# Kernel optimization log

Hardware: AMD Instinct MI355X
Metric: run time of the kernel (lower is better)

## Reference

```python
import jax, jax.numpy as jnp
import numpy as np

NEIGHBORS = 16   # K nearest neighbors per query point
NQUERIES = 4096  # number of sampled query points (npts)
B, N = 8, 16384  # batch, points per cloud


def setup_inputs() -> dict:
    key = jax.random.key(0)
    xyz1 = jax.random.normal(key, (B, N, 3), dtype=jnp.float32)
    return {"xyz1": xyz1}


def _sample_one(xyz, key):
    """Sequential coverage sampling for one point cloud xyz: (n, 3).

    Faithful to indices_conv_reduction: a 'used' counter per point; each
    iteration picks a uniformly-random point among the least-used points
    (TF carries current_id and resets it to min(used) when exhausted; since
    counters only increase, this is exactly equivalent to cur = min(used)
    every step), takes its K nearest neighbors, and bumps their counters
    (+1 for neighbors, +100 extra for the chosen center).
    """
    n = xyz.shape[0]

    def step(used, k):
        cur = jnp.min(used)
        mask = used == cur                      # least-used candidate set
        cnt = jnp.sum(mask)
        r = jax.random.randint(k, (), 0, cnt)   # uniform pick among candidates
        index = jnp.argmax(jnp.cumsum(mask) > r)  # r-th True position
        pt = xyz[index]                          # (3,)
        d = jnp.sum((xyz - pt[None, :]) ** 2, axis=1)  # (n,) squared dists
        _, ids = jax.lax.top_k(-d, NEIGHBORS)    # K nearest, sorted
        used = used.at[ids].add(1)
        used = used.at[index].add(100)
        return used, (ids.astype(jnp.int32), pt)

    keys = jax.random.split(key, NQUERIES)
    _, (ids, pts) = jax.lax.scan(step, jnp.zeros((n,), jnp.int32), keys)
    return ids[:, :, None], pts  # (npts, K, 1) int32, (npts, 3) f32


def reference(xyz1):
    xyz1 = jax.lax.stop_gradient(xyz1)  # matches tf.stop_gradient in original
    b = xyz1.shape[0]
    keys = jax.random.split(jax.random.key(42), b)
    idx, pts = jax.vmap(_sample_one)(xyz1, keys)
    return idx, pts
```

## Files before the change

### kernel.cpp

```cpp
#include <hip/hip_runtime.h>
#include <stdint.h>


namespace {

constexpr int BATCH = 8;
constexpr int NPTS  = 16384;
constexpr int NQ    = 4096;
constexpr int KNN   = 16;
constexpr int BLOCK = 512;
constexpr int CH    = NPTS / BLOCK;
constexpr int NWAVE = BLOCK / 64;
constexpr int FLUSH = 256;
constexpr int NCAND = 128;
constexpr size_t IDX_ELEMS = (size_t)BATCH * NQ * KNN;

__device__ __forceinline__ int swz32(int v) { return v + (v >> 5); }
__device__ __forceinline__ int swz16(int w) { return w + 2 * (w >> 6); }

__device__ __forceinline__ void tf2x32(uint32_t k0, uint32_t k1,
                                       uint32_t x0, uint32_t x1,
                                       uint32_t &o0, uint32_t &o1) {
  uint32_t ks2 = k0 ^ k1 ^ 0x1BD11BDAu;
  x0 += k0; x1 += k1;
#define TFR(r) { x0 += x1; x1 = (x1 << (r)) | (x1 >> (32 - (r))); x1 ^= x0; }
  TFR(13) TFR(15) TFR(26) TFR(6)
  x0 += k1;  x1 += ks2 + 1u;
  TFR(17) TFR(29) TFR(16) TFR(24)
  x0 += ks2; x1 += k0 + 2u;
  TFR(13) TFR(15) TFR(26) TFR(6)
  x0 += k0;  x1 += k1 + 3u;
  TFR(17) TFR(29) TFR(16) TFR(24)
  x0 += k1;  x1 += ks2 + 4u;
  TFR(13) TFR(15) TFR(26) TFR(6)
  x0 += ks2; x1 += k0 + 5u;
#undef TFR
  o0 = x0; o1 = x1;
}

__device__ __forceinline__ void split_child(uint32_t pk0, uint32_t pk1,
                                            uint32_t i, uint32_t &c0, uint32_t &c1) {
  tf2x32(pk0, pk1, 0u, i, c0, c1);
}

__device__ __forceinline__ uint32_t bits32_scalar(uint32_t k0, uint32_t k1) {
  uint32_t a0, a1;
  tf2x32(k0, k1, 0u, 0u, a0, a1);
  return a0 ^ a1;
}

__device__ __forceinline__ uint32_t jax_randint(uint32_t hi, uint32_t lo, uint32_t span) {
  uint32_t mult = 65536u % span;
  mult = (mult * mult) % span;
  return ((hi % span) * mult + (lo % span)) % span;
}

__device__ __forceinline__ uint32_t nth_set_bit(uint32_t m, uint32_t n) {
  uint32_t pos = 0;
  #pragma unroll
  for (int sh = 16; sh > 0; sh >>= 1) {
    uint32_t c = __popc(m & ((1u << sh) - 1u));
    if (n >= c) { n -= c; m >>= sh; pos += sh; }
  }
  return pos;
}

}

__global__ __launch_bounds__(BLOCK, 1)
void snn_sample_kernel(const float* __restrict__ xyz, float* __restrict__ out) {
  const int b    = blockIdx.x;
  const int t    = threadIdx.x;
  const int wave = t >> 6;
  const int lane = t & 63;
  const float INF = __int_as_float(0x7f800000);

  __shared__ __align__(16) uint16_t used[16896];
  __shared__ uint32_t mask[NPTS / 32];
  __shared__ uint32_t waveSum[NWAVE];
  __shared__ uint32_t grpSum[64];
  __shared__ uint32_t pcArr[BLOCK];
  __shared__ uint32_t wvMin[NWAVE];
  __shared__ float    gmins[64];
  __shared__ unsigned long long cnd[NCAND];
  __shared__ uint32_t rngHi[BLOCK];
  __shared__ uint32_t rngLo[BLOCK];
  __shared__ float    sPt[3];
  __shared__ uint32_t sNc, sCur;
  __shared__ __align__(16) uint16_t idxChunk[FLUSH * KNN];
  __shared__ __align__(16) float    ptsChunk[FLUSH * 3];

  float px[CH], py[CH], pz[CH];
  {
    const float* sp = xyz + ((size_t)b * NPTS + (size_t)t * CH) * 3;
    #pragma unroll
    for (int j = 0; j < CH; ++j) {
      px[j] = sp[3 * j + 0];
      py[j] = sp[3 * j + 1];
      pz[j] = sp[3 * j + 2];
    }
  }
  {
    uint32_t* u32p = (uint32_t*)used;
    for (int i = t; i < 16896 / 2; i += BLOCK) u32p[i] = 0u;
  }
  mask[t] = 0xFFFFFFFFu;
  pcArr[t] = (uint32_t)CH;
  if (t < 64) grpSum[t] = 256u;
  if (t < NWAVE) waveSum[t] = (uint32_t)(NPTS / NWAVE);
  if (t == 0) { sNc = 0u; sCur = 0u; }

  uint32_t kb0, kb1;
  split_child(0u, 42u, (uint32_t)b, kb0, kb1);
  __syncthreads();

  for (int s = 0; s < NQ; ++s) {
    if (s != 0 && (s & (FLUSH - 1)) == 0) {
      const int base = s - FLUSH;
      float* po = out + ((size_t)b * NQ + base) * KNN;
      for (int i = t; i < FLUSH * KNN; i += BLOCK) po[i] = (float)idxChunk[i];
      float* pp = out + IDX_ELEMS + ((size_t)b * NQ + base) * 3;
      for (int i = t; i < FLUSH * 3; i += BLOCK) pp[i] = ptsChunk[i];
      __syncthreads();
    }

    if ((s & (BLOCK - 1)) == 0) {
      uint32_t ss = (uint32_t)(s + t);
      uint32_t ks0, ks1, u0, u1, v0, v1;
      split_child(kb0, kb1, ss, ks0, ks1);
      split_child(ks0, ks1, 0u, u0, u1);
      split_child(ks0, ks1, 1u, v0, v1);
      rngHi[t] = bits32_scalar(u0, u1);
      rngLo[t] = bits32_scalar(v0, v1);
      __syncthreads();
    }

    uint32_t ws[NWAVE];
    uint32_t span = 0;
    #pragma unroll
    for (int w = 0; w < NWAVE; ++w) { ws[w] = waveSum[w]; span += ws[w]; }
    uint32_t cur = sCur;

    if (span == 0u) {
      uint32_t uvals[CH / 2];
      uint32_t mn = 0xFFFFFFFFu;
      const uint32_t* up32 = (const uint32_t*)used;
      #pragma unroll
      for (int j = 0; j < CH / 2; ++j) {
        uint32_t w2 = up32[swz32(t * (CH / 2) + j)];
        uvals[j] = w2;
        uint32_t a = w2 & 0xFFFFu, c = w2 >> 16;
        uint32_t m2 = a < c ? a : c;
        mn = m2 < mn ? m2 : mn;
      }
      #pragma unroll
      for (int m = 1; m < 64; m <<= 1) {
        uint32_t o = (uint32_t)__shfl_xor((int)mn, m, 64);
        mn = o < mn ? o : mn;
      }
      if (lane == 0) wvMin[wave] = mn;
      __syncthreads();
      uint32_t c = wvMin[0];
      #pragma unroll
      for (int w = 1; w < NWAVE; ++w) c = wvMin[w] < c ? wvMin[w] : c;
      cur = c;
      if (t == 0) sCur = c;
      uint32_t mw = 0;
      #pragma unroll
      for (int j = 0; j < CH / 2; ++j) {
        uint32_t w2 = uvals[j];
        if ((w2 & 0xFFFFu) == cur) mw |= 1u << (2 * j);
        if ((w2 >> 16)     == cur) mw |= 1u << (2 * j + 1);
      }
      mask[t] = mw;
      uint32_t pc = __popc(mw);
      pcArr[t] = pc;
      uint32_t acc = pc;
      acc += (uint32_t)__shfl_xor((int)acc, 1, 64);
      acc += (uint32_t)__shfl_xor((int)acc, 2, 64);
      acc += (uint32_t)__shfl_xor((int)acc, 4, 64);
      if ((lane & 7) == 0) grpSum[(wave << 3) + (lane >> 3)] = acc;
      acc += (uint32_t)__shfl_xor((int)acc, 8, 64);
      acc += (uint32_t)__shfl_xor((int)acc, 16, 64);
      acc += (uint32_t)__shfl_xor((int)acc, 32, 64);
      if (lane == 0) waveSum[wave] = acc;
      __syncthreads();
      span = 0;
      #pragma unroll
      for (int w = 0; w < NWAVE; ++w) { ws[w] = waveSum[w]; span += ws[w]; }
    }

    const uint32_t r = jax_randint(rngHi[s & (BLOCK - 1)],
                                   rngLo[s & (BLOCK - 1)], span);
    uint32_t preWave = 0;
    #pragma unroll
    for (int w = 0; w < NWAVE; ++w) preWave += (w < wave) ? ws[w] : 0u;
    if (r >= preWave && r < preWave + ws[wave]) {
      const int lg = lane >> 3;
      const int li = lane & 7;
      uint32_t gsv[8];
      #pragma unroll
      for (int g = 0; g < 8; ++g) gsv[g] = grpSum[(wave << 3) + g];
      uint32_t pcv[8];
      #pragma unroll
      for (int u = 0; u < 8; ++u) pcv[u] = pcArr[(wave << 6) + (lg << 3) + u];
      uint32_t base = preWave;
      uint32_t pc = 0;
      #pragma unroll
      for (int g = 0; g < 8; ++g) base += (g < lg) ? gsv[g] : 0u;
      #pragma unroll
      for (int u = 0; u < 8; ++u) {
        base += (u < li) ? pcv[u] : 0u;
        pc = (u == li) ? pcv[u] : pc;
      }
      if (r >= base && r < base + pc) {
        uint32_t mw = mask[t];
        uint32_t pos = nth_set_bit(mw, r - base);
        float sx[16], sy[16], sz[16];
        const bool b4 = (pos & 16u) != 0u;
        #pragma unroll
        for (int i = 0; i < 16; ++i) {
          sx[i] = b4 ? px[i + 16] : px[i];
          sy[i] = b4 ? py[i + 16] : py[i];
          sz[i] = b4 ? pz[i + 16] : pz[i];
        }
        const bool b3 = (pos & 8u) != 0u;
        #pragma unroll
        for (int i = 0; i < 8; ++i) {
          sx[i] = b3 ? sx[i + 8] : sx[i];
          sy[i] = b3 ? sy[i + 8] : sy[i];
          sz[i] = b3 ? sz[i + 8] : sz[i];
        }
        const bool b2 = (pos & 4u) != 0u;
        #pragma unroll
        for (int i = 0; i < 4; ++i) {
          sx[i] = b2 ? sx[i + 4] : sx[i];
          sy[i] = b2 ? sy[i + 4] : sy[i];
          sz[i] = b2 ? sz[i + 4] : sz[i];
        }
        const bool b1 = (pos & 2u) != 0u;
        #pragma unroll
        for (int i = 0; i < 2; ++i) {
          sx[i] = b1 ? sx[i + 2] : sx[i];
          sy[i] = b1 ? sy[i + 2] : sy[i];
          sz[i] = b1 ? sz[i + 2] : sz[i];
        }
        const bool b0 = (pos & 1u) != 0u;
        const float fx = b0 ? sx[1] : sx[0];
        const float fy = b0 ? sy[1] : sy[0];
        const float fz = b0 ? sz[1] : sz[0];
        sPt[0] = fx; sPt[1] = fy; sPt[2] = fz;
        float* pb = &ptsChunk[3 * (s & (FLUSH - 1))];
        pb[0] = fx; pb[1] = fy; pb[2] = fz;
      }
    }
    __syncthreads();
    const float cx = sPt[0], cy = sPt[1], cz = sPt[2];

    float dd[CH];
    float m0 = INF, m1 = INF, m2 = INF, m3 = INF;
    #pragma unroll
    for (int j = 0; j < CH; j += 4) {
      #pragma unroll
      for (int q = 0; q < 4; ++q) {
        float dx = __fsub_rn(px[j + q], cx);
        float dy = __fsub_rn(py[j + q], cy);
        float dz = __fsub_rn(pz[j + q], cz);
        dd[j + q] = __fadd_rn(__fadd_rn(__fmul_rn(dx, dx), __fmul_rn(dy, dy)),
                              __fmul_rn(dz, dz));
      }
      m0 = fminf(m0, dd[j + 0]);
      m1 = fminf(m1, dd[j + 1]);
      m2 = fminf(m2, dd[j + 2]);
      m3 = fminf(m3, dd[j + 3]);
    }
    float g = fminf(fminf(m0, m1), fminf(m2, m3));
    g = fminf(g, __shfl_xor(g, 1, 64));
    g = fminf(g, __shfl_xor(g, 2, 64));
    g = fminf(g, __shfl_xor(g, 4, 64));
    if ((lane & 7) == 0) gmins[wave * 8 + (lane >> 3)] = g;
    __syncthreads();

    float thr;
    {
      const uint32_t gb = __float_as_uint(gmins[lane]);
      uint32_t T = 0u;
      #pragma unroll
      for (int k = 31; k >= 16; --k) {
        uint32_t cand = T | (1u << k);
        unsigned long long m = __ballot(gb < cand);
        if (__popcll(m) < 16) T = cand;
      }
      thr = __uint_as_float(T | 0xFFFFu);
    }

    #pragma unroll
    for (int j = 0; j < CH; ++j) {
      if (dd[j] <= thr) {
        uint32_t pos = atomicAdd(&sNc, 1u);
        if (pos < (uint32_t)NCAND) {
          cnd[pos] = (((unsigned long long)__float_as_uint(dd[j])) << 32)
                     | (uint32_t)(t * CH + j);
        }
      }
    }
    __syncthreads();

    if (wave == 0) {
      uint32_t nc = sNc; if (nc > (uint32_t)NCAND) nc = (uint32_t)NCAND;
      if (lane >= (int)nc) cnd[lane] = ~0ull;
      unsigned long long v = (lane < (int)nc) ? cnd[lane] : ~0ull;
      const bool big = nc > 64u;
      unsigned long long v2 = ~0ull;
      if (big) {
        if (64 + lane >= (int)nc) cnd[64 + lane] = ~0ull;
        v2 = (64 + lane < (int)nc) ? cnd[64 + lane] : ~0ull;
      }
      const uint32_t ncR = (nc + 7u) & ~7u;
      uint32_t rank = 0;
      for (uint32_t j = 0; j < ncR; j += 8u) {
        unsigned long long o0 = cnd[j + 0];
        unsigned long long o1 = cnd[j + 1];
        unsigned long long o2 = cnd[j + 2];
        unsigned long long o3 = cnd[j + 3];
        unsigned long long o4 = cnd[j + 4];
        unsigned long long o5 = cnd[j + 5];
        unsigned long long o6 = cnd[j + 6];
        unsigned long long o7 = cnd[j + 7];
        rank += (uint32_t)(o0 < v) + (uint32_t)(o1 < v)
              + (uint32_t)(o2 < v) + (uint32_t)(o3 < v)
              + (uint32_t)(o4 < v) + (uint32_t)(o5 < v)
              + (uint32_t)(o6 < v) + (uint32_t)(o7 < v);
      }
      uint32_t rank2 = 0;
      if (big) {
        for (uint32_t j = 0; j < ncR; j += 4u) {
          unsigned long long o0 = cnd[j + 0];
          unsigned long long o1 = cnd[j + 1];
          unsigned long long o2 = cnd[j + 2];
          unsigned long long o3 = cnd[j + 3];
          rank2 += (uint32_t)(o0 < v2) + (uint32_t)(o1 < v2)
                 + (uint32_t)(o2 < v2) + (uint32_t)(o3 < v2);
        }
      }
      if (lane == 0) sNc = 0u;
      if (lane < (int)nc && rank < (uint32_t)KNN) {
        uint32_t id = (uint32_t)v;
        idxChunk[((s & (FLUSH - 1)) << 4) + rank] = (uint16_t)id;
        int a16 = swz16((int)id);
        uint32_t old = used[a16];
        used[a16] = (uint16_t)(old + ((rank == 0u) ? 101u : 1u));
        if (old == cur) {
          atomicAnd(&mask[id >> 5], ~(1u << (id & 31u)));
          atomicSub(&waveSum[id >> 11], 1u);
          atomicSub(&grpSum[id >> 8], 1u);
          atomicSub(&pcArr[id >> 5], 1u);
        }
      }
      if (big && 64 + lane < (int)nc && rank2 < (uint32_t)KNN) {
        uint32_t id = (uint32_t)v2;
        idxChunk[((s & (FLUSH - 1)) << 4) + rank2] = (uint16_t)id;
        int a16 = swz16((int)id);
        uint32_t old = used[a16];
        used[a16] = (uint16_t)(old + ((rank2 == 0u) ? 101u : 1u));
        if (old == cur) {
          atomicAnd(&mask[id >> 5], ~(1u << (id & 31u)));
          atomicSub(&waveSum[id >> 11], 1u);
          atomicSub(&grpSum[id >> 8], 1u);
          atomicSub(&pcArr[id >> 5], 1u);
        }
      }
    }
    __syncthreads();
  }

  {
    const int base = NQ - FLUSH;
    float* po = out + ((size_t)b * NQ + base) * KNN;
    for (int i = t; i < FLUSH * KNN; i += BLOCK) po[i] = (float)idxChunk[i];
    float* pp = out + IDX_ELEMS + ((size_t)b * NQ + base) * 3;
    for (int i = t; i < FLUSH * 3; i += BLOCK) pp[i] = ptsChunk[i];
  }
}

extern "C" void kernel_launch(void* const* d_in, const int* in_sizes, int n_in,
                              void* d_out, int out_size, void* d_ws, size_t ws_size,
                              hipStream_t stream) {
  (void)in_sizes; (void)n_in; (void)d_ws; (void)ws_size; (void)out_size;
  const float* xyz = (const float*)d_in[0];
  float* out = (float*)d_out;
  snn_sample_kernel<<<dim3(BATCH), dim3(BLOCK), 0, stream>>>(xyz, out);
}
```

Measured before the change: 14.70 ms.

## Precompute next-step random index table on idle wave to shorten critical path

New measurement: 14.19 ms. -3.5%, faster.

```diff
diff --git a/kernel.cpp b/kernel.cpp
--- a/kernel.cpp
+++ b/kernel.cpp
@@ -85,6 +85,7 @@
   __shared__ unsigned long long cnd[NCAND];
   __shared__ uint32_t rngHi[BLOCK];
   __shared__ uint32_t rngLo[BLOCK];
+  __shared__ uint32_t rTab[33];
   __shared__ float    sPt[3];
   __shared__ uint32_t sNc, sCur;
   __shared__ __align__(16) uint16_t idxChunk[FLUSH * KNN];
@@ -112,6 +113,7 @@
 
   uint32_t kb0, kb1;
   split_child(0u, 42u, (uint32_t)b, kb0, kb1);
+  uint32_t spanPrev = 0u;
   __syncthreads();
 
   for (int s = 0; s < NQ; ++s) {
@@ -140,8 +142,10 @@
     #pragma unroll
     for (int w = 0; w < NWAVE; ++w) { ws[w] = waveSum[w]; span += ws[w]; }
     uint32_t cur = sCur;
+    bool fresh = false;
 
     if (span == 0u) {
+      fresh = true;
       uint32_t uvals[CH / 2];
       uint32_t mn = 0xFFFFFFFFu;
       const uint32_t* up32 = (const uint32_t*)used;
@@ -190,24 +194,30 @@
       for (int w = 0; w < NWAVE; ++w) { ws[w] = waveSum[w]; span += ws[w]; }
     }
 
-    const uint32_t r = jax_randint(rngHi[s & (BLOCK - 1)],
-                                   rngLo[s & (BLOCK - 1)], span);
+    uint32_t r;
+    if (s == 0 || fresh) {
+      r = jax_randint(rngHi[s & (BLOCK - 1)], rngLo[s & (BLOCK - 1)], span);
+    } else {
+      r = rTab[spanPrev - span];
+    }
+    spanPrev = span;
+
     uint32_t preWave = 0;
     #pragma unroll
     for (int w = 0; w < NWAVE; ++w) preWave += (w < wave) ? ws[w] : 0u;
+    const int lg = lane >> 3;
+    const int li = lane & 7;
+    uint32_t gsv[8];
+    #pragma unroll
+    for (int g2 = 0; g2 < 8; ++g2) gsv[g2] = grpSum[(wave << 3) + g2];
+    uint32_t pcv[8];
+    #pragma unroll
+    for (int u = 0; u < 8; ++u) pcv[u] = pcArr[(wave << 6) + (lg << 3) + u];
     if (r >= preWave && r < preWave + ws[wave]) {
-      const int lg = lane >> 3;
-      const int li = lane & 7;
-      uint32_t gsv[8];
-      #pragma unroll
-      for (int g = 0; g < 8; ++g) gsv[g] = grpSum[(wave << 3) + g];
-      uint32_t pcv[8];
-      #pragma unroll
-      for (int u = 0; u < 8; ++u) pcv[u] = pcArr[(wave << 6) + (lg << 3) + u];
       uint32_t base = preWave;
       uint32_t pc = 0;
       #pragma unroll
-      for (int g = 0; g < 8; ++g) base += (g < lg) ? gsv[g] : 0u;
+      for (int g2 = 0; g2 < 8; ++g2) base += (g2 < lg) ? gsv[g2] : 0u;
       #pragma unroll
       for (int u = 0; u < 8; ++u) {
         base += (u < li) ? pcv[u] : 0u;
@@ -358,17 +368,35 @@
         }
       }
       if (big && 64 + lane < (int)nc && rank2 < (uint32_t)KNN) {
-        uint32_t id = (uint32_t)v2;
-        idxChunk[((s & (FLUSH - 1)) << 4) + rank2] = (uint16_t)id;
-        int a16 = swz16((int)id);
-        uint32_t old = used[a16];
-        used[a16] = (uint16_t)(old + ((rank2 == 0u) ? 101u : 1u));
-        if (old == cur) {
-          atomicAnd(&mask[id >> 5], ~(1u << (id & 31u)));
-          atomicSub(&waveSum[id >> 11], 1u);
-          atomicSub(&grpSum[id >> 8], 1u);
-          atomicSub(&pcArr[id >> 5], 1u);
-        }
+        uint32_t id2 = (uint32_t)v2;
+        idxChunk[((s & (FLUSH - 1)) << 4) + rank2] = (uint16_t)id2;
+        int a216 = swz16((int)id2);
+        uint32_t old2 = used[a216];
+        used[a216] = (uint16_t)(old2 + ((rank2 == 0u) ? 101u : 1u));
+        if (old2 == cur) {
+          atomicAnd(&mask[id2 >> 5], ~(1u << (id2 & 31u)));
+          atomicSub(&waveSum[id2 >> 11], 1u);
+          atomicSub(&grpSum[id2 >> 8], 1u);
+          atomicSub(&pcArr[id2 >> 5], 1u);
+        }
+      }
+    } else if (wave == 1 && lane < 33) {
+      uint32_t sn = span - (uint32_t)lane;
+      if (sn != 0u && sn <= (uint32_t)NPTS) {
+        uint32_t nhi, nlo;
+        if (((s + 1) & (BLOCK - 1)) == 0) {
+          uint32_t ss = (uint32_t)(s + 1);
+          uint32_t ks0, ks1, u0, u1, v0, v1;
+          split_child(kb0, kb1, ss, ks0, ks1);
+          split_child(ks0, ks1, 0u, u0, u1);
+          split_child(ks0, ks1, 1u, v0, v1);
+          nhi = bits32_scalar(u0, u1);
+          nlo = bits32_scalar(v0, v1);
+        } else {
+          nhi = rngHi[(s + 1) & (BLOCK - 1)];
+          nlo = rngLo[(s + 1) & (BLOCK - 1)];
+        }
+        rTab[lane] = jax_randint(nhi, nlo, sn);
       }
     }
     __syncthreads();
```
